# Optimization experiments

Hardware: AMD Instinct MI355X
Metric: run time of the kernel (lower is better)

## Reference

```python
import jax, jax.numpy as jnp
import numpy as np

EPS = 1e-3  # keras LayerNormalization default epsilon
D_INNER = 64


def setup_inputs() -> dict:
    key = jax.random.key(0)
    ks = jax.random.split(key, 5)
    B, N, M, C = 4, 1024, 32, 128
    x = jax.random.normal(ks[0], (B, N, M, C), dtype=jnp.float32)
    # Glorot-uniform init bounds
    lim_qk = float(np.sqrt(6.0 / (C + D_INNER)))
    lim_v = float(np.sqrt(6.0 / (C + C)))
    w_q = jax.random.uniform(ks[1], (C, D_INNER), jnp.float32, -lim_qk, lim_qk)
    w_k = jax.random.uniform(ks[2], (C, D_INNER), jnp.float32, -lim_qk, lim_qk)
    w_v = jax.random.uniform(ks[3], (C, C), jnp.float32, -lim_v, lim_v)
    lam = jnp.full((C,), 0.1, dtype=jnp.float32)  # lam_init_eps default eps=0.1
    gamma = jnp.ones((C,), dtype=jnp.float32)
    beta = jnp.zeros((C,), dtype=jnp.float32)
    return {"x": x, "gamma": gamma, "beta": beta, "w_q": w_q, "w_k": w_k,
            "w_v": w_v, "lam": lam}


def reference(x, gamma, beta, w_q, w_k, w_v, lam):
    # LayerNorm over channel axis C
    mean = jnp.mean(x, axis=-1, keepdims=True)
    var = jnp.mean(jnp.square(x - mean), axis=-1, keepdims=True)
    xn = (x - mean) * jax.lax.rsqrt(var + EPS) * gamma + beta  # [B,N,M,C]
    xn = jnp.transpose(xn, (0, 2, 1, 3))  # [B,M,N,C] attention over N per feature
    q = jnp.einsum('bmnc,cd->bmnd', xn, w_q)
    k = jnp.einsum('bmnc,cd->bmnd', xn, w_k)
    scores = jnp.einsum('bmnd,bmkd->bmnk', q, k) / jnp.sqrt(
        jnp.asarray(D_INNER, dtype=jnp.float32))
    A = jax.nn.softmax(scores, axis=-1)  # [B,M,N,N]
    v = jnp.einsum('bmnc,ce->bmne', xn, w_v)  # [B,M,N,C]
    attn = jnp.einsum('bmnk,bmkc->bmnc', A, v)
    attn = jnp.transpose(attn, (0, 2, 1, 3))  # back to [B,N,M,C]
    return x + attn * lam
```

## Files before the change

kernel.cpp:

```cpp
#include <hip/hip_runtime.h>
#include <hip/hip_bf16.h>

#define B_ 4
#define N_ 1024
#define M_ 32
#define C_ 128
#define D_ 64
#define BM_ (B_*M_)

typedef float f32x4 __attribute__((ext_vector_type(4)));
typedef float f32x16 __attribute__((ext_vector_type(16)));
typedef short short8 __attribute__((ext_vector_type(8)));
typedef short short4v __attribute__((ext_vector_type(4)));

#define EXP2(x) __builtin_amdgcn_exp2f(x)

static __device__ __forceinline__ int cvtpk_bf16(float lo, float hi) {
  int r;
  asm volatile("v_cvt_pk_bf16_f32 %0, %1, %2" : "=v"(r) : "v"(lo), "v"(hi));
  return r;
}
static __device__ __forceinline__ void plswap(int& a, int& b) {
  asm volatile("v_permlane32_swap_b32 %0, %1" : "+v"(a), "+v"(b));
}

__global__ __launch_bounds__(256) void prep_weights(
    const float* __restrict__ wq, const float* __restrict__ wk,
    const float* __restrict__ wv, __hip_bfloat16* __restrict__ wt) {
  int idx = blockIdx.x * 256 + threadIdx.x;
  int col = idx >> 7;
  int kk  = idx & 127;
  float v;
  if (col < 64)        v = wq[kk * 64 + col] * (0.125f * 1.44269504088896f);
  else if (col < 128)  v = wk[kk * 64 + (col - 64)];
  else                 v = wv[kk * 128 + (col - 128)];
  wt[col * 128 + kk] = __float2bfloat16(v);
}

__global__ __launch_bounds__(512, 6) void ln_qkv(
    const float* __restrict__ x, const float* __restrict__ gamma,
    const float* __restrict__ beta, const __hip_bfloat16* __restrict__ wt,
    __hip_bfloat16* __restrict__ q, __hip_bfloat16* __restrict__ k,
    __hip_bfloat16* __restrict__ vt) {
  __shared__ alignas(16) __hip_bfloat16 xn[128][136];

  int bid = blockIdx.x;
  int bm  = bid >> 3;
  int n0  = (bid & 7) * 128;
  int b   = bm >> 5, m = bm & 31;
  int tid = threadIdx.x;

  const float* xbase = x + ((((size_t)b * N_ + n0) * M_ + m) * C_);
  int c4 = tid & 31;
  float4 vch[8];
  #pragma unroll
  for (int it = 0; it < 8; ++it) {
    int r = (it * 512 + tid) >> 5;
    vch[it] = *reinterpret_cast<const float4*>(xbase + (size_t)r * (M_ * C_) + c4 * 4);
  }
  float4 g4 = *reinterpret_cast<const float4*>(gamma + c4 * 4);
  float4 b4 = *reinterpret_cast<const float4*>(beta + c4 * 4);

  #pragma unroll
  for (int it = 0; it < 8; ++it) {
    int r = (it * 512 + tid) >> 5;
    float4 v = vch[it];
    float s  = (v.x + v.y) + (v.z + v.w);
    float sq = (v.x * v.x + v.y * v.y) + (v.z * v.z + v.w * v.w);
    s  += __shfl_xor(s, 1);  sq += __shfl_xor(sq, 1);
    s  += __shfl_xor(s, 2);  sq += __shfl_xor(sq, 2);
    s  += __shfl_xor(s, 4);  sq += __shfl_xor(sq, 4);
    s  += __shfl_xor(s, 8);  sq += __shfl_xor(sq, 8);
    s  += __shfl_xor(s, 16); sq += __shfl_xor(sq, 16);
    float mean = s * (1.f / 128.f);
    float var  = sq * (1.f / 128.f) - mean * mean;
    float rstd = rsqrtf(var + 1e-3f);
    alignas(8) __hip_bfloat16 tmp[4];
    tmp[0] = __float2bfloat16((v.x - mean) * rstd * g4.x + b4.x);
    tmp[1] = __float2bfloat16((v.y - mean) * rstd * g4.y + b4.y);
    tmp[2] = __float2bfloat16((v.z - mean) * rstd * g4.z + b4.z);
    tmp[3] = __float2bfloat16((v.w - mean) * rstd * g4.w + b4.w);
    *reinterpret_cast<short4v*>(&xn[r][c4 * 4]) =
        *reinterpret_cast<const short4v*>(tmp);
  }
  __syncthreads();

  int w = tid >> 6, l = tid & 63, lr = l & 15, lh = l >> 4;
  int ct0 = w, ct1 = w + 8;

  short8 wf0[4], wf1[4];
  #pragma unroll
  for (int h = 0; h < 4; ++h) {
    wf0[h] = *reinterpret_cast<const short8*>(
        &wt[(ct0 * 16 + lr) * 128 + h * 32 + lh * 8]);
    wf1[h] = *reinterpret_cast<const short8*>(
        &wt[(ct1 * 16 + lr) * 128 + h * 32 + lh * 8]);
  }

  const f32x4 fzero = {0.f, 0.f, 0.f, 0.f};
  int col0 = ct0 * 16 + lr;
  int cV   = w * 16 + lr;
  #pragma unroll
  for (int rt = 0; rt < 8; ++rt) {
    short8 a[4];
    #pragma unroll
    for (int h = 0; h < 4; ++h)
      a[h] = *reinterpret_cast<const short8*>(&xn[rt * 16 + lr][h * 32 + lh * 8]);
    f32x4 acc0 = fzero, acc1 = fzero;
    #pragma unroll
    for (int h = 0; h < 4; ++h) {
      acc0 = __builtin_amdgcn_mfma_f32_16x16x32_bf16(a[h], wf0[h], acc0, 0, 0, 0);
      acc1 = __builtin_amdgcn_mfma_f32_16x16x32_bf16(a[h], wf1[h], acc1, 0, 0, 0);
    }
    int nb = n0 + rt * 16 + lh * 4;
    if (ct0 < 4) {
      #pragma unroll
      for (int r = 0; r < 4; ++r)
        q[((size_t)bm * N_ + nb + r) * D_ + col0] = __float2bfloat16(acc0[r]);
    } else {
      #pragma unroll
      for (int r = 0; r < 4; ++r)
        k[((size_t)bm * N_ + nb + r) * D_ + (col0 - 64)] = __float2bfloat16(acc0[r]);
    }
    alignas(8) __hip_bfloat16 tmp[4];
    #pragma unroll
    for (int r = 0; r < 4; ++r) tmp[r] = __float2bfloat16(acc1[r]);
    *reinterpret_cast<short4v*>(&vt[((size_t)bm * C_ + cV) * N_ + nb]) =
        *reinterpret_cast<const short4v*>(tmp);
  }
}

__global__ __launch_bounds__(256, 2) void attn_kernel(
    const float* __restrict__ x, const float* __restrict__ lam,
    const __hip_bfloat16* __restrict__ q, const __hip_bfloat16* __restrict__ k,
    const __hip_bfloat16* __restrict__ vt, float* __restrict__ out) {
  __shared__ alignas(16) __hip_bfloat16 kbuf[2][64 * 72];
  __shared__ alignas(16) __hip_bfloat16 vbuf[128 * 72];

  int h   = blockIdx.x;
  int s_  = h >> 3;
  int bm  = (s_ >> 3) * 8 + (h & 7);
  int n0  = (s_ & 7) * 128;
  int b   = bm >> 5, m = bm & 31;
  int tid = threadIdx.x;
  int w = tid >> 6, l = tid & 63;
  int lq = l & 31, hi = l >> 5;

  const __hip_bfloat16* kbase = k + (size_t)bm * N_ * D_;
  const __hip_bfloat16* vbase = vt + (size_t)bm * C_ * N_;

  int kr0 = tid >> 3,          kc = tid & 7;
  int kr1 = (tid + 256) >> 3;
  int vr[4], vc = tid & 7;
  #pragma unroll
  for (int i = 0; i < 4; ++i) vr[i] = (tid + i * 256) >> 3;

  short8 qf[4];
  {
    int n = n0 + w * 32 + lq;
    const __hip_bfloat16* qp = q + ((size_t)bm * N_ + n) * D_;
    #pragma unroll
    for (int s = 0; s < 4; ++s)
      qf[s] = *reinterpret_cast<const short8*>(qp + s * 16 + hi * 8);
  }

  f32x16 acc[4];
  const f32x16 z16 = {0.f,0.f,0.f,0.f,0.f,0.f,0.f,0.f,
                      0.f,0.f,0.f,0.f,0.f,0.f,0.f,0.f};
  #pragma unroll
  for (int ct = 0; ct < 4; ++ct) acc[ct] = z16;
  float m_run = 0.f, l_run = 0.f;

  short8 kreg[2], vreg[4];
  kreg[0] = *reinterpret_cast<const short8*>(&kbase[(size_t)kr0 * D_ + kc * 8]);
  kreg[1] = *reinterpret_cast<const short8*>(&kbase[(size_t)kr1 * D_ + kc * 8]);
  #pragma unroll
  for (int i = 0; i < 4; ++i)
    vreg[i] = *reinterpret_cast<const short8*>(&vbase[(size_t)vr[i] * N_ + vc * 8]);
  *reinterpret_cast<short8*>(&kbuf[0][kr0 * 72 + kc * 8]) = kreg[0];
  *reinterpret_cast<short8*>(&kbuf[0][kr1 * 72 + kc * 8]) = kreg[1];
  #pragma unroll
  for (int i = 0; i < 4; ++i)
    *reinterpret_cast<short8*>(&vbuf[vr[i] * 72 + vc * 8]) = vreg[i];
  __syncthreads();

  for (int t = 0; t < 16; ++t) {
    int cur = t & 1, nxt = cur ^ 1;
    if (t < 15) {
      int j0n = (t + 1) * 64;
      kreg[0] = *reinterpret_cast<const short8*>(&kbase[(size_t)(j0n + kr0) * D_ + kc * 8]);
      kreg[1] = *reinterpret_cast<const short8*>(&kbase[(size_t)(j0n + kr1) * D_ + kc * 8]);
      #pragma unroll
      for (int i = 0; i < 4; ++i)
        vreg[i] = *reinterpret_cast<const short8*>(&vbase[(size_t)vr[i] * N_ + j0n + vc * 8]);
    }

    const __hip_bfloat16* kt = kbuf[cur];

    f32x16 st[2];
    st[0] = z16; st[1] = z16;
    #pragma unroll
    for (int s = 0; s < 4; ++s) {
      short8 kf0 = *reinterpret_cast<const short8*>(&kt[lq * 72 + s * 16 + hi * 8]);
      st[0] = __builtin_amdgcn_mfma_f32_32x32x16_bf16(kf0, qf[s], st[0], 0, 0, 0);
      short8 kf1 = *reinterpret_cast<const short8*>(&kt[(32 + lq) * 72 + s * 16 + hi * 8]);
      st[1] = __builtin_amdgcn_mfma_f32_32x32x16_bf16(kf1, qf[s], st[1], 0, 0, 0);
    }

    float mx;
    {
      float t8[8];
      #pragma unroll
      for (int i = 0; i < 8; ++i)
        t8[i] = fmaxf(fmaxf(st[0][i], st[0][i + 8]), fmaxf(st[1][i], st[1][i + 8]));
      float a0 = fmaxf(fmaxf(t8[0], t8[1]), fmaxf(t8[2], t8[3]));
      float a1 = fmaxf(fmaxf(t8[4], t8[5]), fmaxf(t8[6], t8[7]));
      mx = fmaxf(a0, a1);
      mx = fmaxf(mx, __shfl_xor(mx, 32));
    }

    #pragma unroll
    for (int i = 0; i < 16; ++i) {
      st[0][i] = EXP2(st[0][i] - m_run);
      st[1][i] = EXP2(st[1][i] - m_run);
    }

    if (__any(mx > m_run + 8.0f)) {
      float mnew = fmaxf(m_run, mx);
      float fac = EXP2(m_run - mnew);
      m_run = mnew;
      l_run *= fac;
      #pragma unroll
      for (int i = 0; i < 16; ++i) { st[0][i] *= fac; st[1][i] *= fac; }
      #pragma unroll
      for (int reg = 0; reg < 16; ++reg) {
        int qi = (reg & 3) + 8 * (reg >> 2) + 4 * hi;
        float f = __shfl(fac, qi);
        #pragma unroll
        for (int ct = 0; ct < 4; ++ct) acc[ct][reg] *= f;
      }
    }

    union W4 { int w[4]; short8 s8; } pf[4];
    #pragma unroll
    for (int t32 = 0; t32 < 2; ++t32) {
      int A = cvtpk_bf16(st[t32][0], st[t32][1]);
      int Bw = cvtpk_bf16(st[t32][2], st[t32][3]);
      int Cw = cvtpk_bf16(st[t32][4], st[t32][5]);
      int Dw = cvtpk_bf16(st[t32][6], st[t32][7]);
      plswap(A, Cw);
      plswap(Bw, Dw);
      pf[t32 * 2].w[0] = A;  pf[t32 * 2].w[1] = Bw;
      pf[t32 * 2].w[2] = Cw; pf[t32 * 2].w[3] = Dw;
      int E = cvtpk_bf16(st[t32][8], st[t32][9]);
      int F = cvtpk_bf16(st[t32][10], st[t32][11]);
      int G = cvtpk_bf16(st[t32][12], st[t32][13]);
      int H = cvtpk_bf16(st[t32][14], st[t32][15]);
      plswap(E, G);
      plswap(F, H);
      pf[t32 * 2 + 1].w[0] = E; pf[t32 * 2 + 1].w[1] = F;
      pf[t32 * 2 + 1].w[2] = G; pf[t32 * 2 + 1].w[3] = H;
    }

    if (t < 15) {
      *reinterpret_cast<short8*>(&kbuf[nxt][kr0 * 72 + kc * 8]) = kreg[0];
      *reinterpret_cast<short8*>(&kbuf[nxt][kr1 * 72 + kc * 8]) = kreg[1];
    }

    __syncthreads();

    #pragma unroll
    for (int kb = 0; kb < 4; ++kb) {
      #pragma unroll
      for (int ct = 0; ct < 4; ++ct) {
        short8 vf = *reinterpret_cast<const short8*>(
            &vbuf[(ct * 32 + lq) * 72 + kb * 16 + hi * 8]);
        acc[ct] = __builtin_amdgcn_mfma_f32_32x32x16_bf16(pf[kb].s8, vf, acc[ct], 0, 0, 0);
      }
    }

    {
      float s8[8];
      #pragma unroll
      for (int i = 0; i < 8; ++i)
        s8[i] = (st[0][i] + st[0][i + 8]) + (st[1][i] + st[1][i + 8]);
      float rs = ((s8[0] + s8[1]) + (s8[2] + s8[3])) +
                 ((s8[4] + s8[5]) + (s8[6] + s8[7]));
      rs += __shfl_xor(rs, 32);
      l_run += rs;
    }

    if (t < 15) {
      __syncthreads();
      #pragma unroll
      for (int i = 0; i < 4; ++i)
        *reinterpret_cast<short8*>(&vbuf[vr[i] * 72 + vc * 8]) = vreg[i];
    }
  }

  float inv = 1.0f / l_run;
  float rlv[16];
  #pragma unroll
  for (int reg = 0; reg < 16; ++reg) {
    int qi = (reg & 3) + 8 * (reg >> 2) + 4 * hi;
    rlv[reg] = __shfl(inv, qi);
  }
  #pragma unroll
  for (int ct = 0; ct < 4; ++ct) {
    int c = ct * 32 + lq;
    float lamc = lam[c];
    #pragma unroll
    for (int reg = 0; reg < 16; ++reg) {
      int qi = (reg & 3) + 8 * (reg >> 2) + 4 * hi;
      int n = n0 + w * 32 + qi;
      size_t idx = ((((size_t)b * N_ + n) * M_ + m) * C_) + c;
      out[idx] = x[idx] + acc[ct][reg] * rlv[reg] * lamc;
    }
  }
}

extern "C" void kernel_launch(void* const* d_in, const int* in_sizes, int n_in,
                              void* d_out, int out_size, void* d_ws, size_t ws_size,
                              hipStream_t stream) {
  const float* x     = (const float*)d_in[0];
  const float* gamma = (const float*)d_in[1];
  const float* beta  = (const float*)d_in[2];
  const float* wq    = (const float*)d_in[3];
  const float* wk    = (const float*)d_in[4];
  const float* wv    = (const float*)d_in[5];
  const float* lam   = (const float*)d_in[6];
  float* out = (float*)d_out;

  __hip_bfloat16* ws = (__hip_bfloat16*)d_ws;
  __hip_bfloat16* wt = ws;
  __hip_bfloat16* q  = wt + 256 * 128;
  __hip_bfloat16* k  = q + (size_t)BM_ * N_ * D_;
  __hip_bfloat16* vt = k + (size_t)BM_ * N_ * D_;

  prep_weights<<<128, 256, 0, stream>>>(wq, wk, wv, wt);
  ln_qkv<<<BM_ * (N_ / 128), 512, 0, stream>>>(x, gamma, beta, wt, q, k, vt);
  attn_kernel<<<BM_ * (N_ / 128), 256, 0, stream>>>(x, lam, q, k, vt, out);
}
```

Before: 112.6 us.

## Software-pipeline PV MFMA one tile behind QK with triple-buffered V

Moves the P·V MFMA for tile t-1 so it runs right after the QK MFMAs of tile t, letting the two matrix phases overlap with the softmax work. V tiles are now triple-buffered in LDS, which lets the loop use a single barrier per iteration instead of two. An epilogue handles the last tile's P·V, and the main loop is fully unrolled. In exchange, LDS use roughly doubles and register pressure rises, which may limit occupancy under the 2-blocks-per-CU launch bound, and the full unroll enlarges the code.

```diff
diff --git a/kernel.cpp b/kernel.cpp
--- a/kernel.cpp
+++ b/kernel.cpp
@@ -135,7 +135,7 @@
     const __hip_bfloat16* __restrict__ q, const __hip_bfloat16* __restrict__ k,
     const __hip_bfloat16* __restrict__ vt, float* __restrict__ out) {
   __shared__ alignas(16) __hip_bfloat16 kbuf[2][64 * 72];
-  __shared__ alignas(16) __hip_bfloat16 vbuf[128 * 72];
+  __shared__ alignas(16) __hip_bfloat16 vbuf[3][128 * 72];
 
   int h   = blockIdx.x;
   int s_  = h >> 3;
@@ -171,7 +171,9 @@
   for (int ct = 0; ct < 4; ++ct) acc[ct] = z16;
   float m_run = 0.f, l_run = 0.f;
 
+  union W4 { int w[4]; short8 s8; } pf[4];
   short8 kreg[2], vreg[4];
+
   kreg[0] = *reinterpret_cast<const short8*>(&kbase[(size_t)kr0 * D_ + kc * 8]);
   kreg[1] = *reinterpret_cast<const short8*>(&kbase[(size_t)kr1 * D_ + kc * 8]);
   #pragma unroll
@@ -181,11 +183,15 @@
   *reinterpret_cast<short8*>(&kbuf[0][kr1 * 72 + kc * 8]) = kreg[1];
   #pragma unroll
   for (int i = 0; i < 4; ++i)
-    *reinterpret_cast<short8*>(&vbuf[vr[i] * 72 + vc * 8]) = vreg[i];
+    *reinterpret_cast<short8*>(&vbuf[0][vr[i] * 72 + vc * 8]) = vreg[i];
   __syncthreads();
 
+  #pragma unroll
   for (int t = 0; t < 16; ++t) {
-    int cur = t & 1, nxt = cur ^ 1;
+    int kcur = t & 1, knxt = kcur ^ 1;
+    int vw = (t + 1) % 3;
+    int vrd = (t + 2) % 3;
+
     if (t < 15) {
       int j0n = (t + 1) * 64;
       kreg[0] = *reinterpret_cast<const short8*>(&kbase[(size_t)(j0n + kr0) * D_ + kc * 8]);
@@ -195,7 +201,7 @@
         vreg[i] = *reinterpret_cast<const short8*>(&vbase[(size_t)vr[i] * N_ + j0n + vc * 8]);
     }
 
-    const __hip_bfloat16* kt = kbuf[cur];
+    const __hip_bfloat16* kt = kbuf[kcur];
 
     f32x16 st[2];
     st[0] = z16; st[1] = z16;
@@ -205,6 +211,19 @@
       st[0] = __builtin_amdgcn_mfma_f32_32x32x16_bf16(kf0, qf[s], st[0], 0, 0, 0);
       short8 kf1 = *reinterpret_cast<const short8*>(&kt[(32 + lq) * 72 + s * 16 + hi * 8]);
       st[1] = __builtin_amdgcn_mfma_f32_32x32x16_bf16(kf1, qf[s], st[1], 0, 0, 0);
+    }
+
+    if (t > 0) {
+      const __hip_bfloat16* vtt = vbuf[vrd];
+      #pragma unroll
+      for (int kb = 0; kb < 4; ++kb) {
+        #pragma unroll
+        for (int ct = 0; ct < 4; ++ct) {
+          short8 vf = *reinterpret_cast<const short8*>(
+              &vtt[(ct * 32 + lq) * 72 + kb * 16 + hi * 8]);
+          acc[ct] = __builtin_amdgcn_mfma_f32_32x32x16_bf16(pf[kb].s8, vf, acc[ct], 0, 0, 0);
+        }
+      }
     }
 
     float mx;
@@ -241,7 +260,6 @@
       }
     }
 
-    union W4 { int w[4]; short8 s8; } pf[4];
     #pragma unroll
     for (int t32 = 0; t32 < 2; ++t32) {
       int A = cvtpk_bf16(st[t32][0], st[t32][1]);
@@ -262,23 +280,6 @@
       pf[t32 * 2 + 1].w[2] = G; pf[t32 * 2 + 1].w[3] = H;
     }
 
-    if (t < 15) {
-      *reinterpret_cast<short8*>(&kbuf[nxt][kr0 * 72 + kc * 8]) = kreg[0];
-      *reinterpret_cast<short8*>(&kbuf[nxt][kr1 * 72 + kc * 8]) = kreg[1];
-    }
-
-    __syncthreads();
-
-    #pragma unroll
-    for (int kb = 0; kb < 4; ++kb) {
-      #pragma unroll
-      for (int ct = 0; ct < 4; ++ct) {
-        short8 vf = *reinterpret_cast<const short8*>(
-            &vbuf[(ct * 32 + lq) * 72 + kb * 16 + hi * 8]);
-        acc[ct] = __builtin_amdgcn_mfma_f32_32x32x16_bf16(pf[kb].s8, vf, acc[ct], 0, 0, 0);
-      }
-    }
-
     {
       float s8[8];
       #pragma unroll
@@ -291,10 +292,25 @@
     }
 
     if (t < 15) {
+      *reinterpret_cast<short8*>(&kbuf[knxt][kr0 * 72 + kc * 8]) = kreg[0];
+      *reinterpret_cast<short8*>(&kbuf[knxt][kr1 * 72 + kc * 8]) = kreg[1];
+      #pragma unroll
+      for (int i = 0; i < 4; ++i)
+        *reinterpret_cast<short8*>(&vbuf[vw][vr[i] * 72 + vc * 8]) = vreg[i];
       __syncthreads();
-      #pragma unroll
-      for (int i = 0; i < 4; ++i)
-        *reinterpret_cast<short8*>(&vbuf[vr[i] * 72 + vc * 8]) = vreg[i];
+    }
+  }
+
+  {
+    const __hip_bfloat16* vtt = vbuf[0];
+    #pragma unroll
+    for (int kb = 0; kb < 4; ++kb) {
+      #pragma unroll
+      for (int ct = 0; ct < 4; ++ct) {
+        short8 vf = *reinterpret_cast<const short8*>(
+            &vtt[(ct * 32 + lq) * 72 + kb * 16 + hi * 8]);
+        acc[ct] = __builtin_amdgcn_mfma_f32_32x32x16_bf16(pf[kb].s8, vf, acc[ct], 0, 0, 0);
+      }
     }
   }
 
```

Measured after the change: 112.1 us. No clear change (-0.4%).
